# Optimization experiments

Hardware: AMD Instinct MI355X
Metric: run time of the kernel (lower is better)

Reference implementation:

```python
import jax, jax.numpy as jnp
import numpy as np

N_NODES = 4096
IN_F = 128
HEADS = 8
HIDDEN = 8  # out_features // n_heads = 64 // 8
SLOPE = 0.2


def setup_inputs() -> dict:
    key = jax.random.key(0)
    k1, k2, k3, k4, k5 = jax.random.split(key, 5)
    h = jax.random.normal(k1, (N_NODES, IN_F), dtype=jnp.float32)
    # sparse-ish dense adjacency mask with guaranteed self-loops (avoids empty softmax rows)
    adj = jax.random.bernoulli(k2, 0.02, (N_NODES, N_NODES))
    adj = adj | jnp.eye(N_NODES, dtype=bool)
    adj = adj[:, :, None]  # [n, n, 1] as in the torch module
    W = jax.random.normal(k3, (IN_F, HEADS * HIDDEN), dtype=jnp.float32) * 0.1
    a_l = jax.random.normal(k4, (HIDDEN,), dtype=jnp.float32) * 0.1
    a_r = jax.random.normal(k5, (HIDDEN,), dtype=jnp.float32) * 0.1
    return {"h": h, "adj": adj, "W": W, "a_l": a_l, "a_r": a_r}


def reference(h, adj, W, a_l, a_r):
    n = h.shape[0]
    g = (h @ W).reshape(n, HEADS, HIDDEN)            # [n, h, d]
    # attn([g_i || g_j]) = g_i . a_l + g_j . a_r (shared across heads)
    sl = jnp.einsum('nhd,d->nh', g, a_l)             # [n, h]
    sr = jnp.einsum('nhd,d->nh', g, a_r)             # [n, h]
    e = sl[:, None, :] + sr[None, :, :]              # [n, n, h] (i = dst, j = src)
    e = jnp.where(e >= 0, e, SLOPE * e)              # leaky relu
    mask = adj[:, :, 0]                              # [n, n] bool
    e = jnp.where(mask[:, :, None], e, -jnp.inf)
    a = jax.nn.softmax(e, axis=1)                    # softmax over source nodes j
    out = jnp.einsum('ijh,jhf->ihf', a, g)           # [n, h, d]
    return out.reshape(n, HEADS * HIDDEN)            # is_concat=True
```

## Files before the change

kernel.cpp:

```cpp
#include <hip/hip_runtime.h>
#include <hip/hip_bf16.h>
#include <math.h>

#define N_NODES 4096
#define IN_F    128
#define HEADS   8
#define HIDDEN  8
#define OUTD    64
#define SLOPE   0.2f

__global__ __launch_bounds__(256) void gemm_kernel(
    const void* __restrict__ hraw, const void* __restrict__ Wraw,
    const void* __restrict__ alraw, const void* __restrict__ arraw,
    int* __restrict__ flags,
    float* __restrict__ g, float* __restrict__ slArr, float* __restrict__ srArr) {

    __shared__ float lh[4][IN_F];
    __shared__ float lg[4][OUTD];

    const int tid = threadIdx.x;
    const int n0  = blockIdx.x * 4;

    const __hip_bfloat16* hb = (const __hip_bfloat16*)hraw;
    float p0 = __bfloat162float(hb[tid]);
    float p1 = __bfloat162float(hb[tid + 256]);
    int bad = (!(fabsf(p0) < 1e4f)) | (!(fabsf(p1) < 1e4f));
    unsigned long long bm = __ballot(bad);
    const int isF32 = (bm != 0ULL) ? 1 : 0;
    if (blockIdx.x == 0 && tid == 0) flags[0] = isF32;

    if (isF32) {
        const float2* hf = (const float2*)((const float*)hraw + (size_t)n0 * IN_F);
        ((float2*)&lh[0][0])[tid] = hf[tid];
    } else {
        const ushort2* h2 = (const ushort2*)((const __hip_bfloat16*)hraw + (size_t)n0 * IN_F);
        ushort2 v = h2[tid];
        float2 f;
        f.x = __bfloat162float(*(__hip_bfloat16*)&v.x);
        f.y = __bfloat162float(*(__hip_bfloat16*)&v.y);
        ((float2*)&lh[0][0])[tid] = f;
    }
    __syncthreads();

    const int nn = tid >> 6;
    const int c  = tid & 63;
    float acc = 0.f;
    if (isF32) {
        const float* Wf = (const float*)Wraw;
        #pragma unroll 8
        for (int k = 0; k < IN_F; ++k) acc += lh[nn][k] * Wf[k * OUTD + c];
    } else {
        const __hip_bfloat16* Wb = (const __hip_bfloat16*)Wraw;
        #pragma unroll 8
        for (int k = 0; k < IN_F; ++k) acc += lh[nn][k] * __bfloat162float(Wb[k * OUTD + c]);
    }
    g[(size_t)(n0 + nn) * OUTD + c] = acc;
    lg[nn][c] = acc;
    __syncthreads();

    if (tid < 32) {
        const int m  = tid >> 3;
        const int hh = tid & 7;
        float sl = 0.f, sr = 0.f;
        if (isF32) {
            const float* al = (const float*)alraw;
            const float* ar = (const float*)arraw;
            #pragma unroll
            for (int d = 0; d < HIDDEN; ++d) {
                float gv = lg[m][hh * HIDDEN + d];
                sl += gv * al[d]; sr += gv * ar[d];
            }
        } else {
            const __hip_bfloat16* al = (const __hip_bfloat16*)alraw;
            const __hip_bfloat16* ar = (const __hip_bfloat16*)arraw;
            #pragma unroll
            for (int d = 0; d < HIDDEN; ++d) {
                float gv = lg[m][hh * HIDDEN + d];
                sl += gv * __bfloat162float(al[d]); sr += gv * __bfloat162float(ar[d]);
            }
        }
        slArr[(size_t)(n0 + m) * HEADS + hh] = sl;
        srArr[(size_t)(n0 + m) * HEADS + hh] = sr;
    }
}

__global__ __launch_bounds__(256) void attn_kernel(
    const void* __restrict__ adjraw, const int* __restrict__ flags,
    const float* __restrict__ g,
    const float* __restrict__ slArr, const float* __restrict__ srArr,
    void* __restrict__ outraw) {

    const int i   = blockIdx.x;
    const int tid = threadIdx.x;

    __shared__ int   edges[1024];
    __shared__ int   cnt;
    __shared__ int   byteflag;
    __shared__ float red[4][HEADS * 9];

    if (tid == 0) { cnt = 0; byteflag = 0; }
    __syncthreads();

    {
        const uint4* a4 = (const uint4*)adjraw;
        uint4 d = a4[tid];
        if ((d.x | d.y | d.z | d.w) > 1u) atomicOr(&byteflag, 1);
    }
    __syncthreads();

    if (byteflag) {
        const uint4* arow = (const uint4*)((const unsigned char*)adjraw + (size_t)i * N_NODES);
        uint4 w = arow[tid];
        unsigned int wc[4] = {w.x, w.y, w.z, w.w};
        #pragma unroll
        for (int c = 0; c < 4; ++c) {
            if (wc[c]) {
                #pragma unroll
                for (int b = 0; b < 4; ++b) {
                    if ((wc[c] >> (8 * b)) & 0xFFu) {
                        int p = atomicAdd(&cnt, 1);
                        if (p < 1024) edges[p] = tid * 16 + 4 * c + b;
                    }
                }
            }
        }
    } else {
        const uint4* arow = (const uint4*)((const int*)adjraw + (size_t)i * N_NODES);
        uint4 w0 = arow[tid];
        uint4 w1 = arow[tid + 256];
        uint4 w2 = arow[tid + 512];
        uint4 w3 = arow[tid + 768];
        uint4 ww[4] = {w0, w1, w2, w3};
        #pragma unroll
        for (int it = 0; it < 4; ++it) {
            const int base = it * 1024 + tid * 4;
            uint4 w = ww[it];
            if (w.x) { int p = atomicAdd(&cnt, 1); if (p < 1024) edges[p] = base + 0; }
            if (w.y) { int p = atomicAdd(&cnt, 1); if (p < 1024) edges[p] = base + 1; }
            if (w.z) { int p = atomicAdd(&cnt, 1); if (p < 1024) edges[p] = base + 2; }
            if (w.w) { int p = atomicAdd(&cnt, 1); if (p < 1024) edges[p] = base + 3; }
        }
    }
    __syncthreads();

    const int E = min(cnt, 1024);

    const int lane = tid & 63;
    const int wave = tid >> 6;
    const int hh   = lane & 7;
    const int s    = lane >> 3;
    const int slot = wave * 8 + s;

    const float sl_h = slArr[(size_t)i * HEADS + hh];

    float l = 0.f;
    float o[HIDDEN] = {0.f, 0.f, 0.f, 0.f, 0.f, 0.f, 0.f, 0.f};

    for (int e = slot; e < E; e += 32) {
        int j = edges[e];
        float x = sl_h + srArr[(size_t)j * HEADS + hh];
        x = (x >= 0.f) ? x : SLOPE * x;
        float wgt = __expf(x);
        l += wgt;
        const float4* gp = (const float4*)(g + (size_t)j * OUTD + hh * HIDDEN);
        float4 g0 = gp[0], g1 = gp[1];
        o[0] += wgt * g0.x; o[1] += wgt * g0.y; o[2] += wgt * g0.z; o[3] += wgt * g0.w;
        o[4] += wgt * g1.x; o[5] += wgt * g1.y; o[6] += wgt * g1.z; o[7] += wgt * g1.w;
    }

    #pragma unroll
    for (int m = 8; m < 64; m <<= 1) {
        l += __shfl_xor(l, m, 64);
        #pragma unroll
        for (int d = 0; d < HIDDEN; ++d) o[d] += __shfl_xor(o[d], m, 64);
    }
    if (s == 0) {
        red[wave][hh * 9 + 8] = l;
        #pragma unroll
        for (int d = 0; d < HIDDEN; ++d) red[wave][hh * 9 + d] = o[d];
    }
    __syncthreads();

    if (tid < OUTD) {
        const int h2 = tid >> 3, d2 = tid & 7;
        float os = 0.f, ls = 0.f;
        #pragma unroll
        for (int w = 0; w < 4; ++w) {
            os += red[w][h2 * 9 + d2];
            ls += red[w][h2 * 9 + 8];
        }
        float val = os / ls;
        if (flags[0]) {
            ((float*)outraw)[(size_t)i * OUTD + tid] = val;
        } else {
            ((__hip_bfloat16*)outraw)[(size_t)i * OUTD + tid] = __float2bfloat16(val);
        }
    }
}

extern "C" void kernel_launch(void* const* d_in, const int* in_sizes, int n_in,
                              void* d_out, int out_size, void* d_ws, size_t ws_size,
                              hipStream_t stream) {
    const void* h   = d_in[0];
    const void* adj = d_in[1];
    const void* W   = d_in[2];
    const void* al  = d_in[3];
    const void* ar  = d_in[4];

    char* ws = (char*)d_ws;
    int*   flags = (int*)ws;
    float* g     = (float*)(ws + 256);
    float* slA   = (float*)(ws + 256 + (size_t)N_NODES * OUTD * 4);
    float* srA   = (float*)(ws + 256 + (size_t)N_NODES * OUTD * 4
                                   + (size_t)N_NODES * HEADS * 4);

    gemm_kernel<<<N_NODES / 4, 256, 0, stream>>>(h, W, al, ar, flags, g, slA, srA);
    attn_kernel<<<N_NODES, 256, 0, stream>>>(adj, flags, g, slA, srA, d_out);
}
```

Baseline: 113.3 us.

## Use per-wave ballot edge compaction and hoist adjacency-format detection to gemm kernel

The attention kernel now builds its edge lists per wave, using ballot and popcount prefix sums instead of shared-memory atomics on a block-wide counter. This removes two block barriers and the atomic contention during compaction. The check for whether the adjacency is stored as bytes or ints moves into block 0 of the gemm kernel and is passed through a workspace flag, so attention blocks no longer rescan the adjacency header. The trade-off is that each wave holds at most 320 edges and processes only its own quarter of the row, so rows with more edges in one quarter would be truncated and load across waves can be uneven.

```diff
diff --git a/kernel.cpp b/kernel.cpp
--- a/kernel.cpp
+++ b/kernel.cpp
@@ -8,15 +8,18 @@
 #define HIDDEN  8
 #define OUTD    64
 #define SLOPE   0.2f
+#define SEGCAP  320
 
 __global__ __launch_bounds__(256) void gemm_kernel(
     const void* __restrict__ hraw, const void* __restrict__ Wraw,
     const void* __restrict__ alraw, const void* __restrict__ arraw,
+    const void* __restrict__ adjraw,
     int* __restrict__ flags,
     float* __restrict__ g, float* __restrict__ slArr, float* __restrict__ srArr) {
 
     __shared__ float lh[4][IN_F];
     __shared__ float lg[4][OUTD];
+    __shared__ int   bflag;
 
     const int tid = threadIdx.x;
     const int n0  = blockIdx.x * 4;
@@ -27,7 +30,21 @@
     int bad = (!(fabsf(p0) < 1e4f)) | (!(fabsf(p1) < 1e4f));
     unsigned long long bm = __ballot(bad);
     const int isF32 = (bm != 0ULL) ? 1 : 0;
-    if (blockIdx.x == 0 && tid == 0) flags[0] = isF32;
+
+    unsigned int adjbig = 0;
+    if (blockIdx.x == 0) {
+        if (tid == 0) bflag = 0;
+        const uint4* a4 = (const uint4*)adjraw;
+        uint4 d0 = a4[tid];
+        uint4 d1 = a4[tid + 256];
+        uint4 d2 = a4[tid + 512];
+        uint4 d3 = a4[tid + 768];
+        unsigned int m0 = d0.x | d0.y | d0.z | d0.w;
+        unsigned int m1 = d1.x | d1.y | d1.z | d1.w;
+        unsigned int m2 = d2.x | d2.y | d2.z | d2.w;
+        unsigned int m3 = d3.x | d3.y | d3.z | d3.w;
+        adjbig = ((m0 | m1 | m2 | m3) > 1u);
+    }
 
     if (isF32) {
         const float2* hf = (const float2*)((const float*)hraw + (size_t)n0 * IN_F);
@@ -41,6 +58,11 @@
         ((float2*)&lh[0][0])[tid] = f;
     }
     __syncthreads();
+
+    if (blockIdx.x == 0) {
+        unsigned long long bm2 = __ballot(adjbig != 0);
+        if ((tid & 63) == 0 && bm2 != 0ULL) atomicOr(&bflag, 1);
+    }
 
     const int nn = tid >> 6;
     const int c  = tid & 63;
@@ -57,6 +79,11 @@
     g[(size_t)(n0 + nn) * OUTD + c] = acc;
     lg[nn][c] = acc;
     __syncthreads();
+
+    if (blockIdx.x == 0 && tid == 0) {
+        flags[0] = isF32;
+        flags[1] = bflag;
+    }
 
     if (tid < 32) {
         const int m  = tid >> 3;
@@ -90,74 +117,60 @@
     const float* __restrict__ slArr, const float* __restrict__ srArr,
     void* __restrict__ outraw) {
 
-    const int i   = blockIdx.x;
-    const int tid = threadIdx.x;
-
-    __shared__ int   edges[1024];
-    __shared__ int   cnt;
-    __shared__ int   byteflag;
+    const int i    = blockIdx.x;
+    const int tid  = threadIdx.x;
+    const int wave = tid >> 6;
+    const int lane = tid & 63;
+
+    __shared__ int   edges[4][SEGCAP];
     __shared__ float red[4][HEADS * 9];
 
-    if (tid == 0) { cnt = 0; byteflag = 0; }
-    __syncthreads();
-
-    {
-        const uint4* a4 = (const uint4*)adjraw;
-        uint4 d = a4[tid];
-        if ((d.x | d.y | d.z | d.w) > 1u) atomicOr(&byteflag, 1);
-    }
-    __syncthreads();
-
-    if (byteflag) {
+    const int byteadj = __builtin_amdgcn_readfirstlane(flags[1]);
+    const int isF32   = __builtin_amdgcn_readfirstlane(flags[0]);
+
+    unsigned int fl[16];
+    if (byteadj) {
         const uint4* arow = (const uint4*)((const unsigned char*)adjraw + (size_t)i * N_NODES);
-        uint4 w = arow[tid];
+        uint4 w = arow[wave * 64 + lane];
         unsigned int wc[4] = {w.x, w.y, w.z, w.w};
         #pragma unroll
-        for (int c = 0; c < 4; ++c) {
-            if (wc[c]) {
-                #pragma unroll
-                for (int b = 0; b < 4; ++b) {
-                    if ((wc[c] >> (8 * b)) & 0xFFu) {
-                        int p = atomicAdd(&cnt, 1);
-                        if (p < 1024) edges[p] = tid * 16 + 4 * c + b;
-                    }
-                }
-            }
-        }
+        for (int r = 0; r < 16; ++r) fl[r] = (wc[r >> 2] >> (8 * (r & 3))) & 0xFFu;
     } else {
         const uint4* arow = (const uint4*)((const int*)adjraw + (size_t)i * N_NODES);
-        uint4 w0 = arow[tid];
-        uint4 w1 = arow[tid + 256];
-        uint4 w2 = arow[tid + 512];
-        uint4 w3 = arow[tid + 768];
-        uint4 ww[4] = {w0, w1, w2, w3};
-        #pragma unroll
-        for (int it = 0; it < 4; ++it) {
-            const int base = it * 1024 + tid * 4;
-            uint4 w = ww[it];
-            if (w.x) { int p = atomicAdd(&cnt, 1); if (p < 1024) edges[p] = base + 0; }
-            if (w.y) { int p = atomicAdd(&cnt, 1); if (p < 1024) edges[p] = base + 1; }
-            if (w.z) { int p = atomicAdd(&cnt, 1); if (p < 1024) edges[p] = base + 2; }
-            if (w.w) { int p = atomicAdd(&cnt, 1); if (p < 1024) edges[p] = base + 3; }
-        }
-    }
-    __syncthreads();
-
-    const int E = min(cnt, 1024);
-
-    const int lane = tid & 63;
-    const int wave = tid >> 6;
-    const int hh   = lane & 7;
-    const int s    = lane >> 3;
-    const int slot = wave * 8 + s;
-
+        uint4 w0 = arow[wave * 256 + lane];
+        uint4 w1 = arow[wave * 256 + 64 + lane];
+        uint4 w2 = arow[wave * 256 + 128 + lane];
+        uint4 w3 = arow[wave * 256 + 192 + lane];
+        fl[0]=w0.x; fl[1]=w0.y; fl[2]=w0.z;  fl[3]=w0.w;
+        fl[4]=w1.x; fl[5]=w1.y; fl[6]=w1.z;  fl[7]=w1.w;
+        fl[8]=w2.x; fl[9]=w2.y; fl[10]=w2.z; fl[11]=w2.w;
+        fl[12]=w3.x; fl[13]=w3.y; fl[14]=w3.z; fl[15]=w3.w;
+    }
+
+    const unsigned long long lmask = (1ULL << lane) - 1ULL;
+    int wcnt = 0;
+    #pragma unroll
+    for (int r = 0; r < 16; ++r) {
+        unsigned long long m = __ballot(fl[r] != 0u);
+        if (fl[r]) {
+            int node = byteadj ? (wave * 1024 + lane * 16 + r)
+                               : (wave * 1024 + (r >> 2) * 256 + lane * 4 + (r & 3));
+            int p = wcnt + (int)__popcll(m & lmask);
+            if (p < SEGCAP) edges[wave][p] = node;
+        }
+        wcnt += (int)__popcll(m);
+    }
+    const int myE = min(wcnt, SEGCAP);
+
+    const int hh = lane & 7;
+    const int s  = lane >> 3;
     const float sl_h = slArr[(size_t)i * HEADS + hh];
 
     float l = 0.f;
     float o[HIDDEN] = {0.f, 0.f, 0.f, 0.f, 0.f, 0.f, 0.f, 0.f};
 
-    for (int e = slot; e < E; e += 32) {
-        int j = edges[e];
+    for (int e = s; e < myE; e += 8) {
+        int j = edges[wave][e];
         float x = sl_h + srArr[(size_t)j * HEADS + hh];
         x = (x >= 0.f) ? x : SLOPE * x;
         float wgt = __expf(x);
@@ -190,7 +203,7 @@
             ls += red[w][h2 * 9 + 8];
         }
         float val = os / ls;
-        if (flags[0]) {
+        if (isF32) {
             ((float*)outraw)[(size_t)i * OUTD + tid] = val;
         } else {
             ((__hip_bfloat16*)outraw)[(size_t)i * OUTD + tid] = __float2bfloat16(val);
@@ -214,6 +227,6 @@
     float* srA   = (float*)(ws + 256 + (size_t)N_NODES * OUTD * 4
                                    + (size_t)N_NODES * HEADS * 4);
 
-    gemm_kernel<<<N_NODES / 4, 256, 0, stream>>>(h, W, al, ar, flags, g, slA, srA);
+    gemm_kernel<<<N_NODES / 4, 256, 0, stream>>>(h, W, al, ar, adj, flags, g, slA, srA);
     attn_kernel<<<N_NODES, 256, 0, stream>>>(adj, flags, g, slA, srA, d_out);
 }
```

Measured after the change: 110.8 us. 1.02x faster.
